# Kernel tuning notes

Hardware: AMD Instinct MI355X
Metric: run time of the kernel (lower is better)

## Reference

```python
import jax, jax.numpy as jnp
import numpy as np

N_MODELS = 16
IN_F = 1024
OUT_F = 1024
N_TOK = 8192


def setup_inputs() -> dict:
    key = jax.random.key(0)
    k1, k2, k3, k4 = jax.random.split(key, 4)
    x = jax.random.normal(k1, (N_TOK, IN_F), dtype=jnp.float32)
    idxs = jax.random.randint(k2, (N_TOK,), 0, N_MODELS, dtype=jnp.int64)
    w = jax.random.normal(k3, (N_MODELS, IN_F, OUT_F), dtype=jnp.float32) * 0.02
    b = jax.random.normal(k4, (N_MODELS, OUT_F), dtype=jnp.float32) * 0.02
    return {"x": x, "idxs": idxs, "w": w, "b": b}


def reference(x, idxs, w, b):
    # Equivalent math to the torch loop: for each expert i, tokens with
    # idxs==i get x @ w[i] + b[i]; finally ReLU over all outputs.
    # Loop over the small fixed expert count; selection by mask avoids
    # materializing the [N, E, out] tensor or gathering per-token weights.
    y = jnp.zeros((x.shape[0], w.shape[2]), dtype=x.dtype)
    for i in range(w.shape[0]):
        yi = x @ w[i] + b[i]  # [N, out]
        y = jnp.where((idxs == i)[:, None], yi, y)
    return jax.nn.relu(y)
```

## Files before the change

### kernel.cpp

```cpp
#include <hip/hip_runtime.h>
#include <hip/hip_bf16.h>
#include <stdint.h>

#define N_MODELS 16
#define IN_F 1024
#define OUT_F 1024
#define N_TOK 8192
#define MAX_MT 80

typedef unsigned short u16;
using us4   = __attribute__((ext_vector_type(4))) unsigned short;
using s16x8 = __attribute__((ext_vector_type(8))) short;
using f32x4 = __attribute__((ext_vector_type(4))) float;

__device__ __forceinline__ u16 f2bf(float f) {
    union { float f; uint32_t u; } v;
    v.f = f;
    uint32_t u = v.u;
    u += 0x7fffu + ((u >> 16) & 1u);
    return (u16)(u >> 16);
}

__device__ __forceinline__ void gload16(const u16* g, u16* l) {
    __builtin_amdgcn_global_load_lds(
        (const __attribute__((address_space(1))) void*)g,
        (__attribute__((address_space(3))) void*)l, 16, 0, 0);
}

#define ROW 17
__global__ __launch_bounds__(256)
void setup_kernel(const int* __restrict__ idxs,
                  int* __restrict__ perm,
                  int* __restrict__ offs,
                  int* __restrict__ tile_off)
{
    __shared__ int cnt[256 * ROW];
    __shared__ int offsS[N_MODELS + 1];
    int t = threadIdx.x;

#pragma unroll
    for (int e = 0; e < N_MODELS; ++e) cnt[t * ROW + e] = 0;
    __syncthreads();

    int base = t * 32;
#pragma unroll
    for (int i = 0; i < 32; ++i) cnt[t * ROW + idxs[base + i]] += 1;
    __syncthreads();

#pragma unroll
    for (int s = 1; s < 256; s <<= 1) {
        int v[N_MODELS];
#pragma unroll
        for (int e = 0; e < N_MODELS; ++e)
            v[e] = (t >= s) ? cnt[(t - s) * ROW + e] : 0;
        __syncthreads();
#pragma unroll
        for (int e = 0; e < N_MODELS; ++e)
            cnt[t * ROW + e] += v[e];
        __syncthreads();
    }

    if (t == 0) {
        int o = 0, to = 0;
        for (int e = 0; e < N_MODELS; ++e) {
            int c = cnt[255 * ROW + e];
            offsS[e] = o;
            offs[e] = o; tile_off[e] = to;
            to += (c + 127) >> 7;
            o  += c;
        }
        offsS[N_MODELS] = o;
        offs[N_MODELS] = o; tile_off[N_MODELS] = to;
    }
    __syncthreads();

    int cur[N_MODELS];
#pragma unroll
    for (int e = 0; e < N_MODELS; ++e)
        cur[e] = offsS[e] + ((t > 0) ? cnt[(t - 1) * ROW + e] : 0);
    __syncthreads();
#pragma unroll
    for (int e = 0; e < N_MODELS; ++e) cnt[t * ROW + e] = cur[e];

#pragma unroll
    for (int i = 0; i < 32; ++i) {
        int tok = base + i;
        int e = idxs[tok];
        perm[cnt[t * ROW + e]++] = tok;
    }
}

#define WBLOCKS (16 * 8 * 16)
#define XBLOCKS (MAX_MT * 8)

__global__ __launch_bounds__(256)
void prep_kernel(const float* __restrict__ w, const float* __restrict__ x,
                 const int* __restrict__ perm, const int* __restrict__ offs,
                 const int* __restrict__ tile_off,
                 u16* __restrict__ wT, u16* __restrict__ xg)
{
    __shared__ float shf[64 * 128];
    int t  = threadIdx.x;
    int bx = blockIdx.x;

    if (bx < WBLOCKS) {
        int e  = bx >> 7;
        int nt = (bx >> 4) & 7;
        int kg = bx & 15;
        const float* wp = w + (size_t)e * (IN_F * OUT_F) + (size_t)kg * 64 * OUT_F + nt * 128;

        int n4  = (t & 31) * 4;
        int kr0 = t >> 5;
#pragma unroll
        for (int i = 0; i < 8; ++i) {
            int k = kr0 + i * 8;
            const float4 v = *(const float4*)(wp + (size_t)k * OUT_F + n4);
            *(float4*)(&shf[k * 128 + n4]) = v;
        }
        __syncthreads();

        int n    = t & 127;
        int oct0 = t >> 7;
        u16* ob = wT + ((size_t)(e * 8 + nt)) * 131072 + (size_t)kg * 8192 + n * 8;
#pragma unroll
        for (int i = 0; i < 4; ++i) {
            int ko = oct0 + i * 2;
            float r[8];
#pragma unroll
            for (int j = 0; j < 8; ++j)
                r[j] = shf[(ko * 8 + j) * 128 + n];
            union { us4 s; uint32_t u[2]; } pk0, pk1;
            union { __hip_bfloat162 h; uint32_t u; } c0, c1, c2, c3;
            c0.h = __float22bfloat162_rn(make_float2(r[0], r[1]));
            c1.h = __float22bfloat162_rn(make_float2(r[2], r[3]));
            c2.h = __float22bfloat162_rn(make_float2(r[4], r[5]));
            c3.h = __float22bfloat162_rn(make_float2(r[6], r[7]));
            pk0.u[0] = c0.u; pk0.u[1] = c1.u;
            pk1.u[0] = c2.u; pk1.u[1] = c3.u;
            union { s16x8 v; us4 h[2]; } outv;
            outv.h[0] = pk0.s; outv.h[1] = pk1.s;
            *(s16x8*)(ob + (size_t)ko * 1024) = outv.v;
        }
    } else {
        u16* sh = (u16*)shf;
        int bx2 = bx - WBLOCKS;
        int mt  = bx2 >> 3;
        int kg  = bx2 & 7;
        int total = tile_off[N_MODELS];
        if (mt >= total) return;
        int e = 0;
        while (tile_off[e + 1] <= mt) ++e;
        int s0   = offs[e] + (mt - tile_off[e]) * 128;
        int sEnd = offs[e + 1];
        int r0   = t >> 3;
        int apos = t & 7;
        int toks[4];
#pragma unroll
        for (int i = 0; i < 4; ++i) {
            int r = r0 + i * 32;
            toks[i] = (s0 + r < sEnd) ? perm[s0 + r] : -1;
        }
        u16* outx = xg + (size_t)mt * 32 * 4096;
        for (int kb4 = 0; kb4 < 4; ++kb4) {
            int kb = kg * 4 + kb4;
#pragma unroll
            for (int i = 0; i < 4; ++i) {
                int r = r0 + i * 32;
                int k = kb * 32 + apos * 4;
                float4 v;
                if (toks[i] >= 0) v = *(const float4*)(x + (size_t)toks[i] * IN_F + k);
                else              v = make_float4(0.f, 0.f, 0.f, 0.f);
                us4 pk; pk.x = f2bf(v.x); pk.y = f2bf(v.y); pk.z = f2bf(v.z); pk.w = f2bf(v.w);
                *(us4*)(&sh[(apos >> 1) * 1024 + r * 8 + (apos & 1) * 4]) = pk;
            }
            __syncthreads();
#pragma unroll
            for (int i = 0; i < 2; ++i) {
                int c = t + i * 256;
                *(s16x8*)(outx + (size_t)kb * 4096 + c * 8) = *(const s16x8*)(&sh[c * 8]);
            }
            __syncthreads();
        }
    }
}

__global__ __launch_bounds__(256)
void gemm_kernel(const u16* __restrict__ xg, const u16* __restrict__ wT,
                 const float* __restrict__ bias,
                 const int* __restrict__ perm, const int* __restrict__ offs,
                 const int* __restrict__ tile_off,
                 float* __restrict__ out)
{
    __shared__ u16 As[4096];
    __shared__ u16 Bs[4096];
    __shared__ int   permS[128];
    __shared__ float biasS[128];
    __shared__ int   toS[N_MODELS + 1];

    int t  = threadIdx.x;
    int bt = blockIdx.y;
    int nt = blockIdx.x;

    if (t <= N_MODELS) toS[t] = tile_off[t];
    __syncthreads();
    if (bt >= toS[N_MODELS]) return;

    int e = 0;
    while (toS[e + 1] <= bt) ++e;
    int s0   = offs[e] + (bt - toS[e]) * 128;
    int sEnd = offs[e + 1];
    int mValid = sEnd - s0; if (mValid > 128) mValid = 128;

    if (t < 128) {
        permS[t] = (s0 + t < sEnd) ? perm[s0 + t] : 0;
        biasS[t] = bias[(size_t)e * OUT_F + nt * 128 + t];
    }

    const u16* atile = xg + (size_t)bt * 32 * 4096;
    const u16* btile = wT + ((size_t)(e * 8 + nt)) * 131072;

    int lane = t & 63;
    int wv   = t >> 6;
    int wm   = (wv >> 1) * 64;
    int wn   = (wv & 1) * 64;
    int m    = lane & 15;
    int q    = lane >> 4;

    f32x4 acc[4][4];
#pragma unroll
    for (int i = 0; i < 4; ++i)
#pragma unroll
        for (int j = 0; j < 4; ++j)
            acc[i][j] = (f32x4){0.f, 0.f, 0.f, 0.f};

    int c = wv * 2;

    for (int kb = 0; kb < 32; ++kb) {
        const u16* ga = atile + kb * 4096;
        const u16* gb = btile + kb * 4096;
        gload16(ga + (c    ) * 512 + lane * 8, &As[(c    ) * 512]);
        gload16(ga + (c + 1) * 512 + lane * 8, &As[(c + 1) * 512]);
        gload16(gb + (c    ) * 512 + lane * 8, &Bs[(c    ) * 512]);
        gload16(gb + (c + 1) * 512 + lane * 8, &Bs[(c + 1) * 512]);
        __syncthreads();

        s16x8 af[4], bf[4];
#pragma unroll
        for (int mt2 = 0; mt2 < 4; ++mt2)
            af[mt2] = *(const s16x8*)(&As[q * 1024 + (wm + mt2 * 16 + m) * 8]);
#pragma unroll
        for (int nt2 = 0; nt2 < 4; ++nt2)
            bf[nt2] = *(const s16x8*)(&Bs[q * 1024 + (wn + nt2 * 16 + m) * 8]);
#pragma unroll
        for (int mt2 = 0; mt2 < 4; ++mt2)
#pragma unroll
            for (int nt2 = 0; nt2 < 4; ++nt2)
                acc[mt2][nt2] = __builtin_amdgcn_mfma_f32_16x16x32_bf16(
                    af[mt2], bf[nt2], acc[mt2][nt2], 0, 0, 0);
        __syncthreads();
    }

#pragma unroll
    for (int mt2 = 0; mt2 < 4; ++mt2) {
        int rbase = wm + mt2 * 16 + q * 4;
#pragma unroll
        for (int i = 0; i < 4; ++i) {
            int r = rbase + i;
            if (r < mValid) {
                int tok = permS[r];
                float* orow = out + (size_t)tok * OUT_F + nt * 128;
#pragma unroll
                for (int nt2 = 0; nt2 < 4; ++nt2) {
                    int col = wn + nt2 * 16 + m;
                    float v = acc[mt2][nt2][i] + biasS[col];
                    orow[col] = v > 0.f ? v : 0.f;
                }
            }
        }
    }
}

extern "C" void kernel_launch(void* const* d_in, const int* in_sizes, int n_in,
                              void* d_out, int out_size, void* d_ws, size_t ws_size,
                              hipStream_t stream) {
    const float* x    = (const float*)d_in[0];
    const int*   idxs = (const int*)d_in[1];
    const float* w    = (const float*)d_in[2];
    const float* b    = (const float*)d_in[3];
    float* out = (float*)d_out;

    u16* wT = (u16*)d_ws;
    u16* xg = wT + (size_t)N_MODELS * IN_F * OUT_F;
    int* perm     = (int*)(xg + (size_t)MAX_MT * 32 * 4096);
    int* offs     = perm + N_TOK;
    int* tile_off = offs + (N_MODELS + 1);

    setup_kernel<<<1, 256, 0, stream>>>(idxs, perm, offs, tile_off);
    prep_kernel<<<WBLOCKS + XBLOCKS, 256, 0, stream>>>(w, x, perm, offs, tile_off, wT, xg);
    gemm_kernel<<<dim3(8, MAX_MT), 256, 0, stream>>>(xg, wT, b, perm, offs, tile_off, out);
}
```

Baseline: 184.3 us.

## Overlap routing setup with weight conversion and split x prep into own kernel

Result: no change. 182.8 us (-0.8%).

```diff
diff --git a/kernel.cpp b/kernel.cpp
--- a/kernel.cpp
+++ b/kernel.cpp
@@ -28,158 +28,147 @@
 }
 
 #define ROW 17
+#define WBLOCKS 2048
+
 __global__ __launch_bounds__(256)
-void setup_kernel(const int* __restrict__ idxs,
-                  int* __restrict__ perm,
-                  int* __restrict__ offs,
-                  int* __restrict__ tile_off)
+void wprep_setup_kernel(const float* __restrict__ w,
+                        const int* __restrict__ idxs,
+                        int* __restrict__ perm,
+                        int* __restrict__ offs,
+                        int* __restrict__ tile_off,
+                        u16* __restrict__ wT)
 {
     __shared__ int cnt[256 * ROW];
     __shared__ int offsS[N_MODELS + 1];
-    int t = threadIdx.x;
-
-#pragma unroll
-    for (int e = 0; e < N_MODELS; ++e) cnt[t * ROW + e] = 0;
-    __syncthreads();
-
-    int base = t * 32;
-#pragma unroll
-    for (int i = 0; i < 32; ++i) cnt[t * ROW + idxs[base + i]] += 1;
-    __syncthreads();
-
-#pragma unroll
-    for (int s = 1; s < 256; s <<= 1) {
-        int v[N_MODELS];
-#pragma unroll
-        for (int e = 0; e < N_MODELS; ++e)
-            v[e] = (t >= s) ? cnt[(t - s) * ROW + e] : 0;
-        __syncthreads();
-#pragma unroll
-        for (int e = 0; e < N_MODELS; ++e)
-            cnt[t * ROW + e] += v[e];
-        __syncthreads();
-    }
-
-    if (t == 0) {
-        int o = 0, to = 0;
-        for (int e = 0; e < N_MODELS; ++e) {
-            int c = cnt[255 * ROW + e];
-            offsS[e] = o;
-            offs[e] = o; tile_off[e] = to;
-            to += (c + 127) >> 7;
-            o  += c;
-        }
-        offsS[N_MODELS] = o;
-        offs[N_MODELS] = o; tile_off[N_MODELS] = to;
-    }
-    __syncthreads();
-
-    int cur[N_MODELS];
-#pragma unroll
-    for (int e = 0; e < N_MODELS; ++e)
-        cur[e] = offsS[e] + ((t > 0) ? cnt[(t - 1) * ROW + e] : 0);
-    __syncthreads();
-#pragma unroll
-    for (int e = 0; e < N_MODELS; ++e) cnt[t * ROW + e] = cur[e];
-
-#pragma unroll
-    for (int i = 0; i < 32; ++i) {
-        int tok = base + i;
-        int e = idxs[tok];
-        perm[cnt[t * ROW + e]++] = tok;
-    }
-}
-
-#define WBLOCKS (16 * 8 * 16)
-#define XBLOCKS (MAX_MT * 8)
-
-__global__ __launch_bounds__(256)
-void prep_kernel(const float* __restrict__ w, const float* __restrict__ x,
-                 const int* __restrict__ perm, const int* __restrict__ offs,
-                 const int* __restrict__ tile_off,
-                 u16* __restrict__ wT, u16* __restrict__ xg)
-{
-    __shared__ float shf[64 * 128];
     int t  = threadIdx.x;
     int bx = blockIdx.x;
 
-    if (bx < WBLOCKS) {
-        int e  = bx >> 7;
-        int nt = (bx >> 4) & 7;
-        int kg = bx & 15;
-        const float* wp = w + (size_t)e * (IN_F * OUT_F) + (size_t)kg * 64 * OUT_F + nt * 128;
-
-        int n4  = (t & 31) * 4;
-        int kr0 = t >> 5;
-#pragma unroll
-        for (int i = 0; i < 8; ++i) {
-            int k = kr0 + i * 8;
-            const float4 v = *(const float4*)(wp + (size_t)k * OUT_F + n4);
-            *(float4*)(&shf[k * 128 + n4]) = v;
-        }
-        __syncthreads();
-
-        int n    = t & 127;
-        int oct0 = t >> 7;
-        u16* ob = wT + ((size_t)(e * 8 + nt)) * 131072 + (size_t)kg * 8192 + n * 8;
-#pragma unroll
-        for (int i = 0; i < 4; ++i) {
-            int ko = oct0 + i * 2;
-            float r[8];
-#pragma unroll
-            for (int j = 0; j < 8; ++j)
-                r[j] = shf[(ko * 8 + j) * 128 + n];
-            union { us4 s; uint32_t u[2]; } pk0, pk1;
-            union { __hip_bfloat162 h; uint32_t u; } c0, c1, c2, c3;
-            c0.h = __float22bfloat162_rn(make_float2(r[0], r[1]));
-            c1.h = __float22bfloat162_rn(make_float2(r[2], r[3]));
-            c2.h = __float22bfloat162_rn(make_float2(r[4], r[5]));
-            c3.h = __float22bfloat162_rn(make_float2(r[6], r[7]));
-            pk0.u[0] = c0.u; pk0.u[1] = c1.u;
-            pk1.u[0] = c2.u; pk1.u[1] = c3.u;
-            union { s16x8 v; us4 h[2]; } outv;
-            outv.h[0] = pk0.s; outv.h[1] = pk1.s;
-            *(s16x8*)(ob + (size_t)ko * 1024) = outv.v;
-        }
-    } else {
-        u16* sh = (u16*)shf;
-        int bx2 = bx - WBLOCKS;
-        int mt  = bx2 >> 3;
-        int kg  = bx2 & 7;
-        int total = tile_off[N_MODELS];
-        if (mt >= total) return;
-        int e = 0;
-        while (tile_off[e + 1] <= mt) ++e;
-        int s0   = offs[e] + (mt - tile_off[e]) * 128;
-        int sEnd = offs[e + 1];
-        int r0   = t >> 3;
-        int apos = t & 7;
-        int toks[4];
+    if (bx == 0) {
+#pragma unroll
+        for (int e = 0; e < N_MODELS; ++e) cnt[t * ROW + e] = 0;
+        __syncthreads();
+
+        int base = t * 32;
+#pragma unroll
+        for (int i = 0; i < 32; ++i) cnt[t * ROW + idxs[base + i]] += 1;
+        __syncthreads();
+
+#pragma unroll
+        for (int s = 1; s < 256; s <<= 1) {
+            int v[N_MODELS];
+#pragma unroll
+            for (int e = 0; e < N_MODELS; ++e)
+                v[e] = (t >= s) ? cnt[(t - s) * ROW + e] : 0;
+            __syncthreads();
+#pragma unroll
+            for (int e = 0; e < N_MODELS; ++e)
+                cnt[t * ROW + e] += v[e];
+            __syncthreads();
+        }
+
+        if (t == 0) {
+            int o = 0, to = 0;
+            for (int e = 0; e < N_MODELS; ++e) {
+                int c = cnt[255 * ROW + e];
+                offsS[e] = o;
+                offs[e] = o; tile_off[e] = to;
+                to += (c + 127) >> 7;
+                o  += c;
+            }
+            offsS[N_MODELS] = o;
+            offs[N_MODELS] = o; tile_off[N_MODELS] = to;
+        }
+        __syncthreads();
+
+        int cur[N_MODELS];
+#pragma unroll
+        for (int e = 0; e < N_MODELS; ++e)
+            cur[e] = offsS[e] + ((t > 0) ? cnt[(t - 1) * ROW + e] : 0);
+        __syncthreads();
+#pragma unroll
+        for (int e = 0; e < N_MODELS; ++e) cnt[t * ROW + e] = cur[e];
+
+#pragma unroll
+        for (int i = 0; i < 32; ++i) {
+            int tok = base + i;
+            int e = idxs[tok];
+            perm[cnt[t * ROW + e]++] = tok;
+        }
+        return;
+    }
+
+    int wb = bx - 1;
+    int e  = wb >> 7;
+    int nt = (wb >> 4) & 7;
+    int kg = wb & 15;
+    int n    = t & 127;
+    int half = t >> 7;
+
+    const float* wp = w  + (size_t)e * (IN_F * OUT_F) + (size_t)nt * 128 + n;
+    u16*         ob = wT + ((size_t)(e * 8 + nt)) * 131072 + (size_t)n * 8;
+
+#pragma unroll
+    for (int i = 0; i < 4; ++i) {
+        int kog = kg * 8 + half + i * 2;
+        float r[8];
+#pragma unroll
+        for (int j = 0; j < 8; ++j)
+            r[j] = wp[(size_t)(kog * 8 + j) * OUT_F];
+        union { __hip_bfloat162 h; uint32_t u; } c0, c1, c2, c3;
+        c0.h = __float22bfloat162_rn(make_float2(r[0], r[1]));
+        c1.h = __float22bfloat162_rn(make_float2(r[2], r[3]));
+        c2.h = __float22bfloat162_rn(make_float2(r[4], r[5]));
+        c3.h = __float22bfloat162_rn(make_float2(r[6], r[7]));
+        union { s16x8 v; uint32_t u[4]; } outv;
+        outv.u[0] = c0.u; outv.u[1] = c1.u; outv.u[2] = c2.u; outv.u[3] = c3.u;
+        *(s16x8*)(ob + (size_t)kog * 1024) = outv.v;
+    }
+}
+
+#define XBLOCKS (MAX_MT * 8)
+
+__global__ __launch_bounds__(256)
+void xprep_kernel(const float* __restrict__ x,
+                  const int* __restrict__ perm, const int* __restrict__ offs,
+                  const int* __restrict__ tile_off,
+                  u16* __restrict__ xg)
+{
+    int t  = threadIdx.x;
+    int bx = blockIdx.x;
+    int mt = bx >> 3;
+    int kg = bx & 7;
+    int total = tile_off[N_MODELS];
+    if (mt >= total) return;
+    int e = 0;
+    while (tile_off[e + 1] <= mt) ++e;
+    int s0   = offs[e] + (mt - tile_off[e]) * 128;
+    int sEnd = offs[e + 1];
+
+    int r0   = t >> 3;
+    int apos = t & 7;
+    int q    = apos >> 1;
+    int j0   = (apos & 1) * 4;
+
+    int toks[4];
+#pragma unroll
+    for (int i = 0; i < 4; ++i) {
+        int r = r0 + i * 32;
+        toks[i] = (s0 + r < sEnd) ? perm[s0 + r] : -1;
+    }
+
+    u16* outx = xg + (size_t)mt * 131072;
+#pragma unroll
+    for (int kb4 = 0; kb4 < 4; ++kb4) {
+        int kb = kg * 4 + kb4;
+        int k  = kb * 32 + apos * 4;
 #pragma unroll
         for (int i = 0; i < 4; ++i) {
             int r = r0 + i * 32;
-            toks[i] = (s0 + r < sEnd) ? perm[s0 + r] : -1;
-        }
-        u16* outx = xg + (size_t)mt * 32 * 4096;
-        for (int kb4 = 0; kb4 < 4; ++kb4) {
-            int kb = kg * 4 + kb4;
-#pragma unroll
-            for (int i = 0; i < 4; ++i) {
-                int r = r0 + i * 32;
-                int k = kb * 32 + apos * 4;
-                float4 v;
-                if (toks[i] >= 0) v = *(const float4*)(x + (size_t)toks[i] * IN_F + k);
-                else              v = make_float4(0.f, 0.f, 0.f, 0.f);
-                us4 pk; pk.x = f2bf(v.x); pk.y = f2bf(v.y); pk.z = f2bf(v.z); pk.w = f2bf(v.w);
-                *(us4*)(&sh[(apos >> 1) * 1024 + r * 8 + (apos & 1) * 4]) = pk;
-            }
-            __syncthreads();
-#pragma unroll
-            for (int i = 0; i < 2; ++i) {
-                int c = t + i * 256;
-                *(s16x8*)(outx + (size_t)kb * 4096 + c * 8) = *(const s16x8*)(&sh[c * 8]);
-            }
-            __syncthreads();
+            float4 v;
+            if (toks[i] >= 0) v = *(const float4*)(x + (size_t)toks[i] * IN_F + k);
+            else              v = make_float4(0.f, 0.f, 0.f, 0.f);
+            us4 pk; pk.x = f2bf(v.x); pk.y = f2bf(v.y); pk.z = f2bf(v.z); pk.w = f2bf(v.w);
+            *(us4*)(outx + (size_t)kb * 4096 + (size_t)q * 1024 + r * 8 + j0) = pk;
         }
     }
 }
@@ -295,7 +284,7 @@
     int* offs     = perm + N_TOK;
     int* tile_off = offs + (N_MODELS + 1);
 
-    setup_kernel<<<1, 256, 0, stream>>>(idxs, perm, offs, tile_off);
-    prep_kernel<<<WBLOCKS + XBLOCKS, 256, 0, stream>>>(w, x, perm, offs, tile_off, wT, xg);
+    wprep_setup_kernel<<<WBLOCKS + 1, 256, 0, stream>>>(w, idxs, perm, offs, tile_off, wT);
+    xprep_kernel<<<XBLOCKS, 256, 0, stream>>>(x, perm, offs, tile_off, xg);
     gemm_kernel<<<dim3(8, MAX_MT), 256, 0, stream>>>(xg, wT, b, perm, offs, tile_off, out);
 }
```
